# Performance work log

Hardware: AMD Instinct MI355X
Metric: run time of the kernel (lower is better)

Reference implementation:

```python
import jax, jax.numpy as jnp
import numpy as np

H = 1024
NH = 16
HD = H // NH  # 64

def setup_inputs() -> dict:
    key = jax.random.key(0)
    ks = jax.random.split(key, 6)
    scale = 0.02
    return {
        "hidden_states": jax.random.normal(ks[0], (2, 2048, H), dtype=jnp.float32),
        "Wq": jax.random.normal(ks[1], (H, H), dtype=jnp.float32) * scale,
        "bq": jnp.zeros((H,), dtype=jnp.float32),
        "Wk": jax.random.normal(ks[2], (H, H), dtype=jnp.float32) * scale,
        "bk": jnp.zeros((H,), dtype=jnp.float32),
        "Wv": jax.random.normal(ks[3], (H, H), dtype=jnp.float32) * scale,
        "bv": jnp.zeros((H,), dtype=jnp.float32),
        "Wo": jax.random.normal(ks[4], (H, H), dtype=jnp.float32) * scale,
        "bo": jnp.zeros((H,), dtype=jnp.float32),
    }

def _split_heads(x):
    # [B,S,H] -> [B,NH,S,HD]
    B, S, _ = x.shape
    return x.reshape(B, S, NH, HD).transpose(0, 2, 1, 3)

def reference(hidden_states, Wq, bq, Wk, bk, Wv, bv, Wo, bo):
    # Linear layers: y = x @ W^T + b (torch nn.Linear convention)
    q = _split_heads(hidden_states @ Wq.T + bq)
    k = _split_heads(hidden_states @ Wk.T + bk)
    v = _split_heads(hidden_states @ Wv.T + bv)
    scores = jnp.einsum("bhqd,bhkd->bhqk", q, k) / jnp.sqrt(jnp.float32(HD))
    probs = jax.nn.softmax(scores, axis=-1)  # dropout is identity in eval mode
    ctx = jnp.einsum("bhqk,bhkd->bhqd", probs, v)
    B, _, S, _ = ctx.shape
    ctx = ctx.transpose(0, 2, 1, 3).reshape(B, S, H)
    return ctx @ Wo.T + bo
```

## Files before the change

kernel.cpp:

```cpp
#include <hip/hip_runtime.h>
#include <hip/hip_bf16.h>

#define H_DIM 1024
#define NHEAD 16
#define HDIM  64
#define BATCH 2
#define SEQ   2048
#define MTOT  (BATCH*SEQ)
#define LOG2E 1.4426950408889634f

typedef _Float16 f16x8 __attribute__((ext_vector_type(8)));
typedef float  f32x4  __attribute__((ext_vector_type(4)));
typedef float  f32x16 __attribute__((ext_vector_type(16)));
typedef short  short8 __attribute__((ext_vector_type(8)));
typedef unsigned uint2v __attribute__((ext_vector_type(2)));
typedef unsigned short u16;

static __device__ __forceinline__ u16 f2h(float f) {
  _Float16 h = (_Float16)f;
  return __builtin_bit_cast(u16, h);
}

static __device__ __forceinline__ void load_lds16(const void* g, void* l) {
  __builtin_amdgcn_global_load_lds(
      (const __attribute__((address_space(1))) unsigned int*)g,
      (__attribute__((address_space(3))) unsigned int*)l, 16, 0, 0);
}

#define N8X (MTOT * H_DIM / 8)
#define N8W (H_DIM * H_DIM / 8)

__global__ __launch_bounds__(256) void conv_all(
    const float* __restrict__ x,  const float* __restrict__ Wq,
    const float* __restrict__ Wk, const float* __restrict__ Wv,
    const float* __restrict__ Wo,
    u16* __restrict__ xb, u16* __restrict__ W3, u16* __restrict__ Wo16) {
  int gi = blockIdx.x * 256 + threadIdx.x;
  const float* src;
  u16* dst;
  int ci;
  if (gi < N8X) {
    src = x; dst = xb; ci = gi;
  } else {
    int j = gi - N8X;
    int which = j >> 17;
    ci = j & (N8W - 1);
    src = which == 0 ? Wq : (which == 1 ? Wk : (which == 2 ? Wv : Wo));
    dst = which < 3 ? W3 + (size_t)which * (N8W * 8) : Wo16;
  }
  float4 a = ((const float4*)src)[ci * 2];
  float4 b = ((const float4*)src)[ci * 2 + 1];
  union { u16 u[8]; short8 s; } r;
  r.u[0] = f2h(a.x); r.u[1] = f2h(a.y); r.u[2] = f2h(a.z); r.u[3] = f2h(a.w);
  r.u[4] = f2h(b.x); r.u[5] = f2h(b.y); r.u[6] = f2h(b.z); r.u[7] = f2h(b.w);
  *(short8*)&dst[ci * 8] = r.s;
}

#define BK 32

__global__ __launch_bounds__(256) void gemm_qkv(
    const u16* __restrict__ Xb, const u16* __restrict__ W3,
    const float* __restrict__ bq, const float* __restrict__ bk2,
    const float* __restrict__ bv,
    u16* __restrict__ qp, u16* __restrict__ kp, u16* __restrict__ vp) {
  __shared__ __align__(16) u16 Al[128 * BK];
  __shared__ __align__(16) u16 Bl[128 * BK];
  const int tid = threadIdx.x;
  const int w = tid >> 6, l = tid & 63, lg = l >> 4, lc = l & 15;
  const int wr = w >> 1, wc = w & 1;
  const int m0 = blockIdx.y * 128, n0 = blockIdx.x * 128;
  const int sr = w * 16 + (l >> 2);
  const int sc = (l & 3) * 8;

  f32x4 acc[4][4];
#pragma unroll
  for (int i = 0; i < 4; i++)
#pragma unroll
    for (int j = 0; j < 4; j++) acc[i][j] = (f32x4){0.f, 0.f, 0.f, 0.f};

  for (int k0 = 0; k0 < H_DIM; k0 += BK) {
    __syncthreads();
    load_lds16(&Xb[(size_t)(m0 + sr) * H_DIM + k0 + sc],      &Al[w * 512]);
    load_lds16(&Xb[(size_t)(m0 + 64 + sr) * H_DIM + k0 + sc], &Al[2048 + w * 512]);
    load_lds16(&W3[(size_t)(n0 + sr) * H_DIM + k0 + sc],      &Bl[w * 512]);
    load_lds16(&W3[(size_t)(n0 + 64 + sr) * H_DIM + k0 + sc], &Bl[2048 + w * 512]);
    __syncthreads();

    f16x8 af[4], bfr[4];
#pragma unroll
    for (int mi = 0; mi < 4; mi++)
      af[mi] = *(const f16x8*)&Al[(wr * 64 + mi * 16 + lc) * BK + lg * 8];
#pragma unroll
    for (int nj = 0; nj < 4; nj++)
      bfr[nj] = *(const f16x8*)&Bl[(wc * 64 + nj * 16 + lc) * BK + lg * 8];
#pragma unroll
    for (int mi = 0; mi < 4; mi++)
#pragma unroll
      for (int nj = 0; nj < 4; nj++)
        acc[mi][nj] = __builtin_amdgcn_mfma_f32_16x16x32_f16(af[mi], bfr[nj],
                                                             acc[mi][nj], 0, 0, 0);
  }

  const int np = n0 >> 10;
  u16* outp = np == 0 ? qp : (np == 1 ? kp : vp);
  const float* bias = np == 0 ? bq : (np == 1 ? bk2 : bv);
  const float scale = np == 0 ? (0.125f * LOG2E) : 1.0f;
  const int nc0 = (n0 & 1023) + wc * 64;
  float bvals[4];
#pragma unroll
  for (int nj = 0; nj < 4; nj++) bvals[nj] = bias[nc0 + nj * 16 + lc];
#pragma unroll
  for (int mi = 0; mi < 4; mi++)
#pragma unroll
    for (int nj = 0; nj < 4; nj++)
#pragma unroll
      for (int r = 0; r < 4; r++) {
        int row = m0 + wr * 64 + mi * 16 + lg * 4 + r;
        outp[(size_t)row * 1024 + nc0 + nj * 16 + lc] =
            f2h((acc[mi][nj][r] + bvals[nj]) * scale);
      }
}

__global__ __launch_bounds__(256) void gemm_oproj(
    const u16* __restrict__ A16, const u16* __restrict__ B16,
    const float* __restrict__ bias, float* __restrict__ out) {
  __shared__ __align__(16) u16 Al[128 * BK];
  __shared__ __align__(16) u16 Bl[128 * BK];
  const int tid = threadIdx.x;
  const int w = tid >> 6, l = tid & 63, lg = l >> 4, lc = l & 15;
  const int wr = w >> 1, wc = w & 1;
  const int m0 = blockIdx.y * 128, n0 = blockIdx.x * 128;
  const int sr = w * 16 + (l >> 2);
  const int sc = (l & 3) * 8;

  f32x4 acc[4][4];
#pragma unroll
  for (int i = 0; i < 4; i++)
#pragma unroll
    for (int j = 0; j < 4; j++) acc[i][j] = (f32x4){0.f, 0.f, 0.f, 0.f};

  for (int k0 = 0; k0 < H_DIM; k0 += BK) {
    __syncthreads();
    load_lds16(&A16[(size_t)(m0 + sr) * H_DIM + k0 + sc],      &Al[w * 512]);
    load_lds16(&A16[(size_t)(m0 + 64 + sr) * H_DIM + k0 + sc], &Al[2048 + w * 512]);
    load_lds16(&B16[(size_t)(n0 + sr) * H_DIM + k0 + sc],      &Bl[w * 512]);
    load_lds16(&B16[(size_t)(n0 + 64 + sr) * H_DIM + k0 + sc], &Bl[2048 + w * 512]);
    __syncthreads();

    f16x8 af[4], bfr[4];
#pragma unroll
    for (int mi = 0; mi < 4; mi++)
      af[mi] = *(const f16x8*)&Al[(wr * 64 + mi * 16 + lc) * BK + lg * 8];
#pragma unroll
    for (int nj = 0; nj < 4; nj++)
      bfr[nj] = *(const f16x8*)&Bl[(wc * 64 + nj * 16 + lc) * BK + lg * 8];
#pragma unroll
    for (int mi = 0; mi < 4; mi++)
#pragma unroll
      for (int nj = 0; nj < 4; nj++)
        acc[mi][nj] = __builtin_amdgcn_mfma_f32_16x16x32_f16(af[mi], bfr[nj],
                                                             acc[mi][nj], 0, 0, 0);
  }

  const int nc0 = n0 + wc * 64;
  float bvals[4];
#pragma unroll
  for (int nj = 0; nj < 4; nj++) bvals[nj] = bias[nc0 + nj * 16 + lc];
#pragma unroll
  for (int mi = 0; mi < 4; mi++)
#pragma unroll
    for (int nj = 0; nj < 4; nj++)
#pragma unroll
      for (int r = 0; r < 4; r++) {
        int row = m0 + wr * 64 + mi * 16 + lg * 4 + r;
        out[(size_t)row * 1024 + nc0 + nj * 16 + lc] = acc[mi][nj][r] + bvals[nj];
      }
}

#define KTILES 16

__global__ __launch_bounds__(256, 4) void attn_mfma7(
    const u16* __restrict__ q, const u16* __restrict__ k,
    const u16* __restrict__ v, u16* __restrict__ Opart,
    float* __restrict__ lpart) {
  __shared__ __align__(16) u16 Ks[64 * 64];
  __shared__ __align__(16) u16 Vt[64 * 64];

  const int tid = threadIdx.x;
  const int w = tid >> 6, l = tid & 63;
  const int l31 = l & 31, l5 = l >> 5;
  const int wg = (blockIdx.x & 7) * 128 + (blockIdx.x >> 3);
  const int qt   = wg & 15;
  const int half = (wg >> 4) & 1;
  const int h    = (wg >> 5) & 15;
  const int b    = wg >> 9;
  const size_t row0 = (size_t)b * SEQ;
  const int grow = qt * 128 + w * 32 + l31;

  f16x8 qf[4];
  {
    const u16* qp = q + (row0 + grow) * H_DIM + h * HDIM + 8 * l5;
#pragma unroll
    for (int dc = 0; dc < 4; dc++)
      qf[dc] = *(const f16x8*)(qp + dc * 16);
  }

  const int c1 = tid + 256;
  const u16* ksrc0 = k + (row0 + half * 1024 + (tid >> 3)) * H_DIM + h * HDIM
                       + ((tid & 7) ^ ((tid >> 3) & 7)) * 8;
  const u16* ksrc1 = k + (row0 + half * 1024 + (c1 >> 3)) * H_DIM + h * HDIM
                       + ((c1 & 7) ^ ((c1 >> 3) & 7)) * 8;

  const int vd = tid & 63, ko = tid >> 6;
  const u16* vsrc = v + (row0 + half * 1024 + ko * 8) * H_DIM + h * HDIM + vd;
  const int vwo0 = vd * 64 + ((ko)     ^ (vd & 7)) * 8;
  const int vwo1 = vd * 64 + ((ko + 4) ^ (vd & 7)) * 8;

  uint4 rV0, rV1;
  {
    unsigned a0 = vsrc[0 * H_DIM], a1 = vsrc[1 * H_DIM];
    unsigned a2 = vsrc[2 * H_DIM], a3 = vsrc[3 * H_DIM];
    unsigned a4 = vsrc[4 * H_DIM], a5 = vsrc[5 * H_DIM];
    unsigned a6 = vsrc[6 * H_DIM], a7 = vsrc[7 * H_DIM];
    rV0.x = a0 | (a1 << 16); rV0.y = a2 | (a3 << 16);
    rV0.z = a4 | (a5 << 16); rV0.w = a6 | (a7 << 16);
    const u16* v2 = vsrc + 32 * H_DIM;
    unsigned b0 = v2[0 * H_DIM], b1 = v2[1 * H_DIM];
    unsigned b2 = v2[2 * H_DIM], b3 = v2[3 * H_DIM];
    unsigned b4 = v2[4 * H_DIM], b5 = v2[5 * H_DIM];
    unsigned b6 = v2[6 * H_DIM], b7 = v2[7 * H_DIM];
    rV1.x = b0 | (b1 << 16); rV1.y = b2 | (b3 << 16);
    rV1.z = b4 | (b5 << 16); rV1.w = b6 | (b7 << 16);
  }

  f32x16 Oacc[2];
#pragma unroll
  for (int i = 0; i < 2; i++)
#pragma unroll
    for (int r = 0; r < 16; r++) Oacc[i][r] = 0.f;
  float lS = 0.f;

  for (int t = 0; t < KTILES; ++t) {
    __syncthreads();
    load_lds16(ksrc0, &Ks[w * 512]);
    load_lds16(ksrc1, &Ks[2048 + w * 512]);
    *(uint4*)&Vt[vwo0] = rV0;
    *(uint4*)&Vt[vwo1] = rV1;
    __syncthreads();
    ksrc0 += 64 * H_DIM;
    ksrc1 += 64 * H_DIM;

    if (t + 1 < KTILES) {
      vsrc += 64 * H_DIM;
      unsigned a0 = vsrc[0 * H_DIM], a1 = vsrc[1 * H_DIM];
      unsigned a2 = vsrc[2 * H_DIM], a3 = vsrc[3 * H_DIM];
      unsigned a4 = vsrc[4 * H_DIM], a5 = vsrc[5 * H_DIM];
      unsigned a6 = vsrc[6 * H_DIM], a7 = vsrc[7 * H_DIM];
      rV0.x = a0 | (a1 << 16); rV0.y = a2 | (a3 << 16);
      rV0.z = a4 | (a5 << 16); rV0.w = a6 | (a7 << 16);
      const u16* v2 = vsrc + 32 * H_DIM;
      unsigned b0 = v2[0 * H_DIM], b1 = v2[1 * H_DIM];
      unsigned b2 = v2[2 * H_DIM], b3 = v2[3 * H_DIM];
      unsigned b4 = v2[4 * H_DIM], b5 = v2[5 * H_DIM];
      unsigned b6 = v2[6 * H_DIM], b7 = v2[7 * H_DIM];
      rV1.x = b0 | (b1 << 16); rV1.y = b2 | (b3 << 16);
      rV1.z = b4 | (b5 << 16); rV1.w = b6 | (b7 << 16);
    }

    unsigned pw[2][4][2];
    float ps = 0.f;
#pragma unroll
    for (int kc = 0; kc < 2; kc++) {
      f32x16 s;
#pragma unroll
      for (int r = 0; r < 16; r++) s[r] = 0.f;
      const int key = kc * 32 + l31;
      const int rowb = key * 64, keyx = key & 7;
#pragma unroll
      for (int dc = 0; dc < 4; dc++) {
        f16x8 af = *(const f16x8*)&Ks[rowb + (((dc << 1) + l5) ^ keyx) * 8];
        s = __builtin_amdgcn_mfma_f32_32x32x16_f16(af, qf[dc], s, 0, 0, 0);
      }
#pragma unroll
      for (int rh = 0; rh < 4; rh++)
#pragma unroll
        for (int k1 = 0; k1 < 2; k1++) {
          float e0 = exp2f(s[4 * rh + 2 * k1]);
          float e1 = exp2f(s[4 * rh + 2 * k1 + 1]);
          ps += e0 + e1;
          pw[kc][rh][k1] = __builtin_bit_cast(
              unsigned, __builtin_amdgcn_cvt_pkrtz(e0, e1));
        }
    }
    lS += ps;

#pragma unroll
    for (int kcc = 0; kcc < 4; kcc++) {
      union { unsigned u[4]; f16x8 v8; } bf;
      const int kcs = kcc >> 1, rhA = (kcc & 1) << 1;
#pragma unroll
      for (int k1 = 0; k1 < 2; k1++) {
        uint2v xy = __builtin_amdgcn_permlane32_swap(
            pw[kcs][rhA][k1], pw[kcs][rhA + 1][k1], false, false);
        bf.u[k1] = xy.x;
        bf.u[2 + k1] = xy.y;
      }
#pragma unroll
      for (int dc2 = 0; dc2 < 2; dc2++) {
        const int d = dc2 * 32 + l31;
        f16x8 vf = *(const f16x8*)&Vt[d * 64 + (((kcc << 1) + l5) ^ (d & 7)) * 8];
        Oacc[dc2] = __builtin_amdgcn_mfma_f32_32x32x16_f16(vf, bf.v8,
                                                           Oacc[dc2], 0, 0, 0);
      }
    }
  }

  lS += __shfl_xor(lS, 32);
  u16* ob = Opart + ((size_t)half * MTOT + row0 + grow) * H_DIM + h * HDIM;
#pragma unroll
  for (int dc2 = 0; dc2 < 2; dc2++)
#pragma unroll
    for (int rh = 0; rh < 4; rh++) {
      int d0 = dc2 * 32 + 8 * rh + 4 * l5;
      uint2 pd;
      pd.x = __builtin_bit_cast(unsigned, __builtin_amdgcn_cvt_pkrtz(
          Oacc[dc2][4 * rh + 0], Oacc[dc2][4 * rh + 1]));
      pd.y = __builtin_bit_cast(unsigned, __builtin_amdgcn_cvt_pkrtz(
          Oacc[dc2][4 * rh + 2], Oacc[dc2][4 * rh + 3]));
      *(uint2*)&ob[d0] = pd;
    }
  if (l < 32)
    lpart[((size_t)half * NHEAD + h) * MTOT + row0 + grow] = lS;
}

__global__ __launch_bounds__(256) void combine_kernel(
    const u16* __restrict__ Opart, const float* __restrict__ lpart,
    u16* __restrict__ ctx) {
  int gi = blockIdx.x * 256 + threadIdx.x;
  int r  = gi >> 7;
  int d0 = (gi & 127) * 8;
  int hh = d0 >> 6;
  float lt = lpart[(size_t)hh * MTOT + r] + lpart[(size_t)(NHEAD + hh) * MTOT + r];
  float inv = 1.f / lt;
  short8 a = *(const short8*)&Opart[(size_t)r * H_DIM + d0];
  short8 c = *(const short8*)&Opart[(size_t)MTOT * H_DIM + (size_t)r * H_DIM + d0];
  union { u16 u[8]; short8 s; } rr;
#pragma unroll
  for (int j = 0; j < 8; j++) {
    float fa = (float)__builtin_bit_cast(_Float16, (u16)a[j]);
    float fc = (float)__builtin_bit_cast(_Float16, (u16)c[j]);
    rr.u[j] = f2h((fa + fc) * inv);
  }
  *(short8*)&ctx[(size_t)gi * 8] = rr.s;
}

extern "C" void kernel_launch(void* const* d_in, const int* in_sizes, int n_in,
                              void* d_out, int out_size, void* d_ws, size_t ws_size,
                              hipStream_t stream) {
  const float* x  = (const float*)d_in[0];
  const float* Wq = (const float*)d_in[1];
  const float* bq = (const float*)d_in[2];
  const float* Wk = (const float*)d_in[3];
  const float* bk = (const float*)d_in[4];
  const float* Wv = (const float*)d_in[5];
  const float* bv = (const float*)d_in[6];
  const float* Wo = (const float*)d_in[7];
  const float* bo = (const float*)d_in[8];
  float* out = (float*)d_out;

  const size_t PL = (size_t)MTOT * H_DIM;
  const size_t WN = (size_t)H_DIM * H_DIM;
  u16* xb    = (u16*)d_ws;
  u16* W3    = xb + PL;
  u16* qp    = W3 + 3 * WN;
  u16* kp    = qp + PL;
  u16* vp    = kp + PL;
  u16* ctxp  = vp + PL;
  u16* Wo16  = ctxp + PL;
  u16* Opart = Wo16 + WN;
  float* lpart = (float*)(Opart + 2 * PL);

  conv_all<<<(N8X + 4 * N8W) / 256, 256, 0, stream>>>(
      x, Wq, Wk, Wv, Wo, xb, W3, Wo16);

  gemm_qkv<<<dim3(3072 / 128, MTOT / 128), 256, 0, stream>>>(
      xb, W3, bq, bk, bv, qp, kp, vp);

  attn_mfma7<<<dim3(1024), 256, 0, stream>>>(qp, kp, vp, Opart, lpart);

  combine_kernel<<<dim3((MTOT * H_DIM / 8) / 256), 256, 0, stream>>>(
      Opart, lpart, ctxp);

  gemm_oproj<<<dim3(1024 / 128, MTOT / 128), 256, 0, stream>>>(
      ctxp, Wo16, bo, out);
}
```

Before: 137.4 us.

## Merge split-KV attention halves into one workgroup and combine through LDS

The attention kernel now runs both key halves for a query tile in a single 512-thread workgroup, one 256-thread group per half, each with its own K/V LDS buffers. After the loop, half 1 writes its partial output and row sums to LDS, and half 0 adds them, normalises and writes the final context directly. This removes the separate combine kernel along with the global round trip for the partial outputs and sums. In exchange, both halves now share every __syncthreads barrier, and the larger workgroup may change occupancy and scheduling.

```diff
diff --git a/kernel.cpp b/kernel.cpp
--- a/kernel.cpp
+++ b/kernel.cpp
@@ -19,6 +19,9 @@
 static __device__ __forceinline__ u16 f2h(float f) {
   _Float16 h = (_Float16)f;
   return __builtin_bit_cast(u16, h);
+}
+static __device__ __forceinline__ float h2f(unsigned bits) {
+  return (float)__builtin_bit_cast(_Float16, (u16)(bits & 0xffffu));
 }
 
 static __device__ __forceinline__ void load_lds16(const void* g, void* l) {
@@ -179,21 +182,23 @@
 
 #define KTILES 16
 
-__global__ __launch_bounds__(256, 4) void attn_mfma7(
+__global__ __launch_bounds__(512, 2) void attn_mfma11(
     const u16* __restrict__ q, const u16* __restrict__ k,
-    const u16* __restrict__ v, u16* __restrict__ Opart,
-    float* __restrict__ lpart) {
-  __shared__ __align__(16) u16 Ks[64 * 64];
-  __shared__ __align__(16) u16 Vt[64 * 64];
+    const u16* __restrict__ v, u16* __restrict__ ctx) {
+  __shared__ __align__(16) u16 Ks[2][64 * 64];
+  __shared__ __align__(16) u16 Vt[2][64 * 64];
 
   const int tid = threadIdx.x;
-  const int w = tid >> 6, l = tid & 63;
+  const int w8 = tid >> 6;
+  const int half = w8 >> 2;
+  const int w = w8 & 3;
+  const int l = tid & 63;
   const int l31 = l & 31, l5 = l >> 5;
-  const int wg = (blockIdx.x & 7) * 128 + (blockIdx.x >> 3);
-  const int qt   = wg & 15;
-  const int half = (wg >> 4) & 1;
-  const int h    = (wg >> 5) & 15;
-  const int b    = wg >> 9;
+  const int ht = tid & 255;
+  const int wg = (blockIdx.x & 7) * 64 + (blockIdx.x >> 3);
+  const int qt = wg & 15;
+  const int h  = (wg >> 4) & 15;
+  const int b  = wg >> 8;
   const size_t row0 = (size_t)b * SEQ;
   const int grow = qt * 128 + w * 32 + l31;
 
@@ -205,13 +210,13 @@
       qf[dc] = *(const f16x8*)(qp + dc * 16);
   }
 
-  const int c1 = tid + 256;
-  const u16* ksrc0 = k + (row0 + half * 1024 + (tid >> 3)) * H_DIM + h * HDIM
-                       + ((tid & 7) ^ ((tid >> 3) & 7)) * 8;
+  const int c1 = ht + 256;
+  const u16* ksrc0 = k + (row0 + half * 1024 + (ht >> 3)) * H_DIM + h * HDIM
+                       + ((ht & 7) ^ ((ht >> 3) & 7)) * 8;
   const u16* ksrc1 = k + (row0 + half * 1024 + (c1 >> 3)) * H_DIM + h * HDIM
                        + ((c1 & 7) ^ ((c1 >> 3) & 7)) * 8;
 
-  const int vd = tid & 63, ko = tid >> 6;
+  const int vd = ht & 63, ko = ht >> 6;
   const u16* vsrc = v + (row0 + half * 1024 + ko * 8) * H_DIM + h * HDIM + vd;
   const int vwo0 = vd * 64 + ((ko)     ^ (vd & 7)) * 8;
   const int vwo1 = vd * 64 + ((ko + 4) ^ (vd & 7)) * 8;
@@ -242,10 +247,10 @@
 
   for (int t = 0; t < KTILES; ++t) {
     __syncthreads();
-    load_lds16(ksrc0, &Ks[w * 512]);
-    load_lds16(ksrc1, &Ks[2048 + w * 512]);
-    *(uint4*)&Vt[vwo0] = rV0;
-    *(uint4*)&Vt[vwo1] = rV1;
+    load_lds16(ksrc0, &Ks[half][w * 512]);
+    load_lds16(ksrc1, &Ks[half][2048 + w * 512]);
+    *(uint4*)&Vt[half][vwo0] = rV0;
+    *(uint4*)&Vt[half][vwo1] = rV1;
     __syncthreads();
     ksrc0 += 64 * H_DIM;
     ksrc1 += 64 * H_DIM;
@@ -278,7 +283,7 @@
       const int rowb = key * 64, keyx = key & 7;
 #pragma unroll
       for (int dc = 0; dc < 4; dc++) {
-        f16x8 af = *(const f16x8*)&Ks[rowb + (((dc << 1) + l5) ^ keyx) * 8];
+        f16x8 af = *(const f16x8*)&Ks[half][rowb + (((dc << 1) + l5) ^ keyx) * 8];
         s = __builtin_amdgcn_mfma_f32_32x32x16_f16(af, qf[dc], s, 0, 0, 0);
       }
 #pragma unroll
@@ -308,50 +313,54 @@
 #pragma unroll
       for (int dc2 = 0; dc2 < 2; dc2++) {
         const int d = dc2 * 32 + l31;
-        f16x8 vf = *(const f16x8*)&Vt[d * 64 + (((kcc << 1) + l5) ^ (d & 7)) * 8];
+        f16x8 vf = *(const f16x8*)&Vt[half][d * 64 + (((kcc << 1) + l5) ^ (d & 7)) * 8];
         Oacc[dc2] = __builtin_amdgcn_mfma_f32_32x32x16_f16(vf, bf.v8,
                                                            Oacc[dc2], 0, 0, 0);
       }
     }
   }
 
+  __syncthreads();
   lS += __shfl_xor(lS, 32);
-  u16* ob = Opart + ((size_t)half * MTOT + row0 + grow) * H_DIM + h * HDIM;
-#pragma unroll
-  for (int dc2 = 0; dc2 < 2; dc2++)
-#pragma unroll
-    for (int rh = 0; rh < 4; rh++) {
-      int d0 = dc2 * 32 + 8 * rh + 4 * l5;
-      uint2 pd;
-      pd.x = __builtin_bit_cast(unsigned, __builtin_amdgcn_cvt_pkrtz(
-          Oacc[dc2][4 * rh + 0], Oacc[dc2][4 * rh + 1]));
-      pd.y = __builtin_bit_cast(unsigned, __builtin_amdgcn_cvt_pkrtz(
-          Oacc[dc2][4 * rh + 2], Oacc[dc2][4 * rh + 3]));
-      *(uint2*)&ob[d0] = pd;
-    }
-  if (l < 32)
-    lpart[((size_t)half * NHEAD + h) * MTOT + row0 + grow] = lS;
-}
-
-__global__ __launch_bounds__(256) void combine_kernel(
-    const u16* __restrict__ Opart, const float* __restrict__ lpart,
-    u16* __restrict__ ctx) {
-  int gi = blockIdx.x * 256 + threadIdx.x;
-  int r  = gi >> 7;
-  int d0 = (gi & 127) * 8;
-  int hh = d0 >> 6;
-  float lt = lpart[(size_t)hh * MTOT + r] + lpart[(size_t)(NHEAD + hh) * MTOT + r];
-  float inv = 1.f / lt;
-  short8 a = *(const short8*)&Opart[(size_t)r * H_DIM + d0];
-  short8 c = *(const short8*)&Opart[(size_t)MTOT * H_DIM + (size_t)r * H_DIM + d0];
-  union { u16 u[8]; short8 s; } rr;
-#pragma unroll
-  for (int j = 0; j < 8; j++) {
-    float fa = (float)__builtin_bit_cast(_Float16, (u16)a[j]);
-    float fc = (float)__builtin_bit_cast(_Float16, (u16)c[j]);
-    rr.u[j] = f2h((fa + fc) * inv);
-  }
-  *(short8*)&ctx[(size_t)gi * 8] = rr.s;
+  const int qloc = w * 32 + l31;
+  u16* ExO = &Ks[0][0];
+  float* ExL = (float*)&Vt[0][0];
+
+  if (half == 1) {
+#pragma unroll
+    for (int dc2 = 0; dc2 < 2; dc2++)
+#pragma unroll
+      for (int rh = 0; rh < 4; rh++) {
+        uint2 pd;
+        pd.x = __builtin_bit_cast(unsigned, __builtin_amdgcn_cvt_pkrtz(
+            Oacc[dc2][4 * rh + 0], Oacc[dc2][4 * rh + 1]));
+        pd.y = __builtin_bit_cast(unsigned, __builtin_amdgcn_cvt_pkrtz(
+            Oacc[dc2][4 * rh + 2], Oacc[dc2][4 * rh + 3]));
+        const int chunk = dc2 * 4 + rh;
+        *(uint2*)&ExO[qloc * 64 + ((chunk ^ (qloc & 7)) << 3) + 4 * l5] = pd;
+      }
+    if (l < 32) ExL[qloc] = lS;
+  }
+  __syncthreads();
+  if (half == 0) {
+    float inv = 1.f / (lS + ExL[qloc]);
+    const size_t obase = (row0 + grow) * H_DIM + h * HDIM;
+#pragma unroll
+    for (int dc2 = 0; dc2 < 2; dc2++)
+#pragma unroll
+      for (int rh = 0; rh < 4; rh++) {
+        const int chunk = dc2 * 4 + rh;
+        uint2 t = *(const uint2*)&ExO[qloc * 64 + ((chunk ^ (qloc & 7)) << 3) + 4 * l5];
+        float o0 = (Oacc[dc2][4 * rh + 0] + h2f(t.x)) * inv;
+        float o1 = (Oacc[dc2][4 * rh + 1] + h2f(t.x >> 16)) * inv;
+        float o2 = (Oacc[dc2][4 * rh + 2] + h2f(t.y)) * inv;
+        float o3 = (Oacc[dc2][4 * rh + 3] + h2f(t.y >> 16)) * inv;
+        uint2 pd;
+        pd.x = __builtin_bit_cast(unsigned, __builtin_amdgcn_cvt_pkrtz(o0, o1));
+        pd.y = __builtin_bit_cast(unsigned, __builtin_amdgcn_cvt_pkrtz(o2, o3));
+        *(uint2*)&ctx[obase + dc2 * 32 + 8 * rh + 4 * l5] = pd;
+      }
+  }
 }
 
 extern "C" void kernel_launch(void* const* d_in, const int* in_sizes, int n_in,
@@ -377,8 +386,6 @@
   u16* vp    = kp + PL;
   u16* ctxp  = vp + PL;
   u16* Wo16  = ctxp + PL;
-  u16* Opart = Wo16 + WN;
-  float* lpart = (float*)(Opart + 2 * PL);
 
   conv_all<<<(N8X + 4 * N8W) / 256, 256, 0, stream>>>(
       x, Wq, Wk, Wv, Wo, xb, W3, Wo16);
@@ -386,10 +393,7 @@
   gemm_qkv<<<dim3(3072 / 128, MTOT / 128), 256, 0, stream>>>(
       xb, W3, bq, bk, bv, qp, kp, vp);
 
-  attn_mfma7<<<dim3(1024), 256, 0, stream>>>(qp, kp, vp, Opart, lpart);
-
-  combine_kernel<<<dim3((MTOT * H_DIM / 8) / 256), 256, 0, stream>>>(
-      Opart, lpart, ctxp);
+  attn_mfma11<<<dim3(512), 512, 0, stream>>>(qp, kp, vp, ctxp);
 
   gemm_oproj<<<dim3(1024 / 128, MTOT / 128), 256, 0, stream>>>(
       ctxp, Wo16, bo, out);
```

Measured after the change: 133.1 us. -3.1%, faster.
